# Kernel optimization log

Measured on AMD Instinct MI355X. Metric: run time of the kernel, lower is better.

## Reference

```python
import jax, jax.numpy as jnp
import numpy as np

BLOCK_SIZE = 256
N_EMBD = 384
NUM_BLOCKS = 3
N_HEADS = 6
VOCAB_SIZE = 65
HEAD = N_EMBD // N_HEADS
EPS = 1e-5


def setup_inputs() -> dict:
    key = jax.random.key(0)
    ks = jax.random.split(key, 20)
    B, T = 64, 256
    s = 0.02
    L = NUM_BLOCKS
    inp = {
        "idx": jax.random.randint(ks[0], (B, T), 0, VOCAB_SIZE),
        "tok_emb": jax.random.normal(ks[1], (VOCAB_SIZE, N_EMBD), jnp.float32) * s,
        "pos_emb": jax.random.normal(ks[2], (BLOCK_SIZE, N_EMBD), jnp.float32) * s,
        "Wq": jax.random.normal(ks[3], (L, N_EMBD, N_EMBD), jnp.float32) * s,
        "Wk": jax.random.normal(ks[4], (L, N_EMBD, N_EMBD), jnp.float32) * s,
        "Wv": jax.random.normal(ks[5], (L, N_EMBD, N_EMBD), jnp.float32) * s,
        "Wo": jax.random.normal(ks[6], (L, N_EMBD, N_EMBD), jnp.float32) * s,
        "bo": jnp.zeros((L, N_EMBD), jnp.float32),
        "ln1_g": jnp.ones((L, N_EMBD), jnp.float32),
        "ln1_b": jnp.zeros((L, N_EMBD), jnp.float32),
        "ln2_g": jnp.ones((L, N_EMBD), jnp.float32),
        "ln2_b": jnp.zeros((L, N_EMBD), jnp.float32),
        "W1": jax.random.normal(ks[7], (L, N_EMBD, 4 * N_EMBD), jnp.float32) * s,
        "b1": jnp.zeros((L, 4 * N_EMBD), jnp.float32),
        "W2": jax.random.normal(ks[8], (L, 4 * N_EMBD, N_EMBD), jnp.float32) * s,
        "b2": jnp.zeros((L, N_EMBD), jnp.float32),
        "lnf_g": jnp.ones((N_EMBD,), jnp.float32),
        "lnf_b": jnp.zeros((N_EMBD,), jnp.float32),
        "Wlm": jax.random.normal(ks[9], (N_EMBD, VOCAB_SIZE), jnp.float32) * s,
        "blm": jnp.zeros((VOCAB_SIZE,), jnp.float32),
    }
    return inp


def _ln(x, g, b):
    m = jnp.mean(x, axis=-1, keepdims=True)
    v = jnp.mean((x - m) ** 2, axis=-1, keepdims=True)
    return (x - m) * jax.lax.rsqrt(v + EPS) * g + b


def reference(idx, tok_emb, pos_emb, Wq, Wk, Wv, Wo, bo, ln1_g, ln1_b,
              ln2_g, ln2_b, W1, b1, W2, b2, lnf_g, lnf_b, Wlm, blm):
    B, T = idx.shape
    x = tok_emb[idx] + pos_emb[:T]  # [B,T,C]
    scale = N_EMBD ** (-0.5)  # NOTE: original scales by full C=N_EMBD, not head_size
    causal = jnp.tril(jnp.ones((T, T), bool))
    neg_inf = jnp.finfo(x.dtype).min
    for l in range(NUM_BLOCKS):
        h = _ln(x, ln1_g[l], ln1_b[l])
        q = (h @ Wq[l]).reshape(B, T, N_HEADS, HEAD)
        k = (h @ Wk[l]).reshape(B, T, N_HEADS, HEAD)
        v = (h @ Wv[l]).reshape(B, T, N_HEADS, HEAD)
        wei = jnp.einsum("bthd,bshd->bhts", q, k) * scale
        wei = jnp.where(causal, wei, neg_inf)
        wei = jax.nn.softmax(wei, axis=-1)  # dropout is identity in eval
        att = jnp.einsum("bhts,bshd->bthd", wei, v).reshape(B, T, N_EMBD)
        x = x + att @ Wo[l] + bo[l]
        h2 = _ln(x, ln2_g[l], ln2_b[l])
        x = x + jax.nn.relu(h2 @ W1[l] + b1[l]) @ W2[l] + b2[l]
    x = _ln(x, lnf_g, lnf_b)
    logits = x @ Wlm + blm  # [B,T,V]
    return logits
```

## Files before the change

kernel.cpp:

```cpp
#include <hip/hip_runtime.h>

#define Bb 64
#define Tt 256
#define Cc 384
#define Ll 3
#define Hh 6
#define HD 64
#define Vv 65
#define FF 1536
#define NT (Bb*Tt)
#define CQ 1152
#define LDP 72

typedef unsigned short u16;
typedef unsigned int   u32;
typedef __attribute__((ext_vector_type(8))) short bf16x8;
typedef __attribute__((ext_vector_type(4))) float f32x4;

__device__ __forceinline__ float bf2f(u16 u) {
    u32 v = ((u32)u) << 16; float f; __builtin_memcpy(&f, &v, 4); return f;
}
__device__ __forceinline__ u16 f2bf(float f) {
    u32 u; __builtin_memcpy(&u, &f, 4);
    u = (u + 0x7fffu + ((u >> 16) & 1u)) >> 16;
    return (u16)u;
}
__device__ __forceinline__ void gload16(const void* g, void* l) {
    __builtin_amdgcn_global_load_lds(
        (const __attribute__((address_space(1))) u32*)g,
        (__attribute__((address_space(3))) u32*)l, 16, 0, 0);
}

__global__ void k_embed(const int* __restrict__ idx, const float* __restrict__ tok,
                        const float* __restrict__ pos, float* __restrict__ x)
{
    long i = (long)blockIdx.x * 256 + threadIdx.x;
    if (i >= (long)NT * Cc) return;
    int c  = (int)(i % Cc);
    int bt = (int)(i / Cc);
    int t  = bt % Tt;
    x[i] = tok[idx[bt] * Cc + c] + pos[t * Cc + c];
}

__global__ __launch_bounds__(256) void k_ln(const float* __restrict__ x,
    const float* __restrict__ g, const float* __restrict__ b, u16* __restrict__ h)
{
    int row  = (int)((blockIdx.x * 256 + threadIdx.x) >> 6);
    int lane = threadIdx.x & 63;
    const float* xr = x + (long)row * Cc;
    float v[6]; float s = 0.f;
    #pragma unroll
    for (int j = 0; j < 6; ++j) { v[j] = xr[lane + 64 * j]; s += v[j]; }
    #pragma unroll
    for (int m = 32; m; m >>= 1) s += __shfl_xor(s, m, 64);
    float mean = s * (1.f / 384.f);
    float q = 0.f;
    #pragma unroll
    for (int j = 0; j < 6; ++j) { float d = v[j] - mean; q += d * d; }
    #pragma unroll
    for (int m = 32; m; m >>= 1) q += __shfl_xor(q, m, 64);
    float rstd = rsqrtf(q * (1.f / 384.f) + 1e-5f);
    u16* hr = h + (long)row * Cc;
    #pragma unroll
    for (int j = 0; j < 6; ++j) {
        int c = lane + 64 * j;
        hr[c] = f2bf((v[j] - mean) * rstd * g[c] + b[c]);
    }
}

__global__ __launch_bounds__(256) void k_cvtT_all(
    const float* __restrict__ Wq, const float* __restrict__ Wk,
    const float* __restrict__ Wv, const float* __restrict__ Wo,
    const float* __restrict__ W1, const float* __restrict__ W2,
    u16* __restrict__ Wqkvt, u16* __restrict__ Wot,
    u16* __restrict__ W1t, u16* __restrict__ W2t)
{
    int t = blockIdx.x;
    const float* src; u16* dst; int K, N, tt;
    if (t < 1728) {
        int m = t / 144; tt = t % 144; K = Cc; N = Cc;
        if (m < 9) {
            int l = m / 3, q = m % 3;
            src = (q == 0 ? Wq : q == 1 ? Wk : Wv) + (size_t)l * Cc * Cc;
            dst = Wqkvt + (size_t)l * CQ * Cc + (size_t)q * Cc * Cc;
        } else {
            int l = m - 9;
            src = Wo + (size_t)l * Cc * Cc;
            dst = Wot + (size_t)l * Cc * Cc;
        }
    } else if (t < 3456) {
        int u = t - 1728; int l = u / 576; tt = u % 576; K = Cc; N = FF;
        src = W1 + (size_t)l * Cc * FF; dst = W1t + (size_t)l * FF * Cc;
    } else {
        int u = t - 3456; int l = u / 576; tt = u % 576; K = FF; N = Cc;
        src = W2 + (size_t)l * FF * Cc; dst = W2t + (size_t)l * Cc * FF;
    }
    int nk = K / 32;
    int kt = (tt % nk) * 32, nt = (tt / nk) * 32;
    __shared__ u16 tile[32][33];
    int tx = threadIdx.x & 31, ty = threadIdx.x >> 5;
    #pragma unroll
    for (int r = 0; r < 4; ++r)
        tile[ty + 8 * r][tx] = f2bf(src[(long)(kt + ty + 8 * r) * N + nt + tx]);
    __syncthreads();
    #pragma unroll
    for (int r = 0; r < 4; ++r)
        dst[(long)(nt + ty + 8 * r) * K + kt + tx] = tile[tx][ty + 8 * r];
}

__global__ void k_cvtT_lm(const float* __restrict__ W, u16* __restrict__ Wt)
{
    int i = blockIdx.x * 256 + threadIdx.x;
    if (i >= 128 * Cc) return;
    int k = i % Cc, n = i / Cc;
    Wt[i] = (n < Vv) ? f2bf(W[(long)k * Vv + n]) : (u16)0;
}

template<int EPI>
__global__ __launch_bounds__(256) void k_gemm128(
    const u16* __restrict__ A, const u16* __restrict__ Bt,
    const float* __restrict__ bias, const float* __restrict__ R,
    void* __restrict__ Cout, int M, int N, int K, int Nout)
{
    __shared__ __align__(16) u16 As[128 * 64];
    __shared__ __align__(16) u16 Bs[128 * 64];
    const int bm = blockIdx.x * 128;
    const int bn = blockIdx.y * 128;
    const int tid = threadIdx.x;
    const int lane = tid & 63, w = tid >> 6;
    const int wr = w >> 1, wc = w & 1;
    const int l15 = lane & 15, g = lane >> 4;
    const int lr = lane >> 3;
    const int lc = ((lane & 7) ^ lr) * 8;

    f32x4 acc[4][4] = {};
    const u16* Ag = A  + (long)(bm + w * 32 + lr) * K + lc;
    const u16* Bg = Bt + (long)(bn + w * 32 + lr) * K + lc;
    u16* Ad = As + (w * 4) * 512;
    u16* Bd = Bs + (w * 4) * 512;

    for (int k0 = 0; k0 < K; k0 += 64) {
        #pragma unroll
        for (int s = 0; s < 4; ++s) {
            gload16(Ag + (long)s * 8 * K + k0, Ad + s * 512);
            gload16(Bg + (long)s * 8 * K + k0, Bd + s * 512);
        }
        __syncthreads();
        #pragma unroll
        for (int h = 0; h < 2; ++h) {
            const int cs = h * 4 + g;
            bf16x8 af[4], bfr[4];
            #pragma unroll
            for (int mi = 0; mi < 4; ++mi) {
                int row = wr * 64 + mi * 16 + l15;
                af[mi] = *(const bf16x8*)((const char*)As + row * 128 + ((cs ^ (row & 7)) << 4));
            }
            #pragma unroll
            for (int ni = 0; ni < 4; ++ni) {
                int row = wc * 64 + ni * 16 + l15;
                bfr[ni] = *(const bf16x8*)((const char*)Bs + row * 128 + ((cs ^ (row & 7)) << 4));
            }
            #pragma unroll
            for (int mi = 0; mi < 4; ++mi)
            #pragma unroll
            for (int ni = 0; ni < 4; ++ni)
                acc[mi][ni] = __builtin_amdgcn_mfma_f32_16x16x32_bf16(af[mi], bfr[ni], acc[mi][ni], 0, 0, 0);
        }
        __syncthreads();
    }
    #pragma unroll
    for (int mi = 0; mi < 4; ++mi)
    #pragma unroll
    for (int ni = 0; ni < 4; ++ni)
    #pragma unroll
    for (int i = 0; i < 4; ++i) {
        int row = bm + wr * 64 + mi * 16 + g * 4 + i;
        int col = bn + wc * 64 + ni * 16 + l15;
        float v = acc[mi][ni][i];
        if constexpr (EPI == 0) {
            ((u16*)Cout)[(long)row * N + col] = f2bf(v);
        } else if constexpr (EPI == 1) {
            v = fmaxf(v + bias[col], 0.f);
            ((u16*)Cout)[(long)row * N + col] = f2bf(v);
        } else if constexpr (EPI == 2) {
            long o = (long)row * N + col;
            ((float*)Cout)[o] = v + bias[col] + R[o];
        } else {
            if (col < Nout)
                ((float*)Cout)[(long)row * Nout + col] = v + bias[col];
        }
    }
}

template<int EPI>
__global__ __launch_bounds__(256) void k_gemm_n64(
    const u16* __restrict__ A, const u16* __restrict__ Bt,
    const float* __restrict__ bias, const float* __restrict__ R,
    void* __restrict__ Cout, int M, int N, int K, int Nout)
{
    __shared__ __align__(16) u16 As[128 * 64];
    __shared__ __align__(16) u16 Bs[64 * 64];
    const int bm = blockIdx.x * 128;
    const int bn = blockIdx.y * 64;
    const int tid = threadIdx.x;
    const int lane = tid & 63, w = tid >> 6;
    const int l15 = lane & 15, g = lane >> 4;
    const int lr = lane >> 3;
    const int lc = ((lane & 7) ^ lr) * 8;

    f32x4 acc[2][4] = {};
    const u16* Ag = A  + (long)(bm + w * 32 + lr) * K + lc;
    const u16* Bg = Bt + (long)(bn + w * 16 + lr) * K + lc;
    u16* Ad = As + (w * 4) * 512;
    u16* Bd = Bs + (w * 2) * 512;

    for (int k0 = 0; k0 < K; k0 += 64) {
        #pragma unroll
        for (int s = 0; s < 4; ++s)
            gload16(Ag + (long)s * 8 * K + k0, Ad + s * 512);
        #pragma unroll
        for (int t = 0; t < 2; ++t)
            gload16(Bg + (long)t * 8 * K + k0, Bd + t * 512);
        __syncthreads();
        #pragma unroll
        for (int h = 0; h < 2; ++h) {
            const int cs = h * 4 + g;
            bf16x8 af[2], bfr[4];
            #pragma unroll
            for (int mi = 0; mi < 2; ++mi) {
                int row = w * 32 + mi * 16 + l15;
                af[mi] = *(const bf16x8*)((const char*)As + row * 128 + ((cs ^ (row & 7)) << 4));
            }
            #pragma unroll
            for (int ni = 0; ni < 4; ++ni) {
                int row = ni * 16 + l15;
                bfr[ni] = *(const bf16x8*)((const char*)Bs + row * 128 + ((cs ^ (row & 7)) << 4));
            }
            #pragma unroll
            for (int mi = 0; mi < 2; ++mi)
            #pragma unroll
            for (int ni = 0; ni < 4; ++ni)
                acc[mi][ni] = __builtin_amdgcn_mfma_f32_16x16x32_bf16(af[mi], bfr[ni], acc[mi][ni], 0, 0, 0);
        }
        __syncthreads();
    }
    #pragma unroll
    for (int mi = 0; mi < 2; ++mi)
    #pragma unroll
    for (int ni = 0; ni < 4; ++ni)
    #pragma unroll
    for (int i = 0; i < 4; ++i) {
        int row = bm + w * 32 + mi * 16 + g * 4 + i;
        int col = bn + ni * 16 + l15;
        float v = acc[mi][ni][i];
        if constexpr (EPI == 0) {
            ((u16*)Cout)[(long)row * N + col] = f2bf(v);
        } else if constexpr (EPI == 1) {
            v = fmaxf(v + bias[col], 0.f);
            ((u16*)Cout)[(long)row * N + col] = f2bf(v);
        } else if constexpr (EPI == 2) {
            long o = (long)row * N + col;
            ((float*)Cout)[o] = v + bias[col] + R[o];
        } else {
            if (col < Nout)
                ((float*)Cout)[(long)row * Nout + col] = v + bias[col];
        }
    }
}

__global__ __launch_bounds__(256) void k_attn_mfma(const u16* __restrict__ qkv,
                                                   u16* __restrict__ att)
{
    __shared__ __align__(16) u16 ks[64][LDP];
    __shared__ __align__(16) u16 vt[64][LDP];
    __shared__ __align__(16) u16 pt[4][16][LDP];
    const int qt = blockIdx.x, hh = blockIdx.y, b = blockIdx.z;
    const int tid = threadIdx.x, lane = tid & 63, w = tid >> 6;
    const int l15 = lane & 15, g = lane >> 4;
    const int q0 = qt * 64;
    const long tokbase = (long)b * Tt;
    const float scale = 0.051031036307982884f;

    bf16x8 qa0, qa1;
    {
        const u16* qp = qkv + (tokbase + q0 + w * 16 + l15) * CQ + hh * HD + g * 8;
        qa0 = *(const bf16x8*)(qp);
        qa1 = *(const bf16x8*)(qp + 32);
    }
    f32x4 o[4] = {};
    float mrow[4] = {-1e30f, -1e30f, -1e30f, -1e30f};
    float lrow[4] = {0.f, 0.f, 0.f, 0.f};

    for (int kt = 0; kt <= qt; ++kt) {
        {
            int key = tid >> 2, c0 = (tid & 3) * 16;
            const u16* kg = qkv + (tokbase + kt * 64 + key) * CQ + Cc     + hh * HD + c0;
            const u16* vg = qkv + (tokbase + kt * 64 + key) * CQ + 2 * Cc + hh * HD + c0;
            *(bf16x8*)&ks[key][c0]     = *(const bf16x8*)kg;
            *(bf16x8*)&ks[key][c0 + 8] = *(const bf16x8*)(kg + 8);
            bf16x8 v0 = *(const bf16x8*)vg;
            bf16x8 v1 = *(const bf16x8*)(vg + 8);
            #pragma unroll
            for (int j = 0; j < 8; ++j) vt[c0 + j][key]     = (u16)v0[j];
            #pragma unroll
            for (int j = 0; j < 8; ++j) vt[c0 + 8 + j][key] = (u16)v1[j];
        }
        __syncthreads();
        f32x4 s[4] = {};
        #pragma unroll
        for (int c = 0; c < 4; ++c) {
            bf16x8 kb0 = *(const bf16x8*)&ks[c * 16 + l15][g * 8];
            bf16x8 kb1 = *(const bf16x8*)&ks[c * 16 + l15][32 + g * 8];
            s[c] = __builtin_amdgcn_mfma_f32_16x16x32_bf16(qa0, kb0, s[c], 0, 0, 0);
            s[c] = __builtin_amdgcn_mfma_f32_16x16x32_bf16(qa1, kb1, s[c], 0, 0, 0);
        }
        const bool diag = (kt == qt);
        #pragma unroll
        for (int c = 0; c < 4; ++c)
        #pragma unroll
        for (int i = 0; i < 4; ++i) {
            float v = s[c][i] * scale;
            if (diag && (c * 16 + l15 > w * 16 + 4 * g + i)) v = -1e30f;
            s[c][i] = v;
        }
        #pragma unroll
        for (int i = 0; i < 4; ++i) {
            float m0 = fmaxf(fmaxf(s[0][i], s[1][i]), fmaxf(s[2][i], s[3][i]));
            #pragma unroll
            for (int mm = 1; mm < 16; mm <<= 1) m0 = fmaxf(m0, __shfl_xor(m0, mm, 64));
            float mn = fmaxf(mrow[i], m0);
            float alpha = __expf(mrow[i] - mn);
            mrow[i] = mn;
            float sum = 0.f;
            #pragma unroll
            for (int c = 0; c < 4; ++c) {
                float p = __expf(s[c][i] - mn);
                s[c][i] = p;
                sum += p;
            }
            #pragma unroll
            for (int mm = 1; mm < 16; mm <<= 1) sum += __shfl_xor(sum, mm, 64);
            lrow[i] = lrow[i] * alpha + sum;
            #pragma unroll
            for (int d = 0; d < 4; ++d) o[d][i] *= alpha;
        }
        #pragma unroll
        for (int c = 0; c < 4; ++c)
        #pragma unroll
        for (int i = 0; i < 4; ++i)
            pt[w][g * 4 + i][c * 16 + l15] = f2bf(s[c][i]);
        bf16x8 pa0 = *(const bf16x8*)&pt[w][l15][g * 8];
        bf16x8 pa1 = *(const bf16x8*)&pt[w][l15][32 + g * 8];
        #pragma unroll
        for (int d = 0; d < 4; ++d) {
            bf16x8 vb0 = *(const bf16x8*)&vt[d * 16 + l15][g * 8];
            bf16x8 vb1 = *(const bf16x8*)&vt[d * 16 + l15][32 + g * 8];
            o[d] = __builtin_amdgcn_mfma_f32_16x16x32_bf16(pa0, vb0, o[d], 0, 0, 0);
            o[d] = __builtin_amdgcn_mfma_f32_16x16x32_bf16(pa1, vb1, o[d], 0, 0, 0);
        }
        __syncthreads();
    }
    #pragma unroll
    for (int i = 0; i < 4; ++i) {
        float inv = 1.f / lrow[i];
        int row = q0 + w * 16 + g * 4 + i;
        u16* ap = att + (tokbase + row) * Cc + hh * HD;
        #pragma unroll
        for (int d = 0; d < 4; ++d)
            ap[d * 16 + l15] = f2bf(o[d][i] * inv);
    }
}

extern "C" void kernel_launch(void* const* d_in, const int* in_sizes, int n_in,
                              void* d_out, int out_size, void* d_ws, size_t ws_size,
                              hipStream_t stream)
{
    (void)in_sizes; (void)n_in; (void)out_size; (void)ws_size;
    const int*   idx  = (const int*)d_in[0];
    const float* tok  = (const float*)d_in[1];
    const float* pos  = (const float*)d_in[2];
    const float* Wq   = (const float*)d_in[3];
    const float* Wk   = (const float*)d_in[4];
    const float* Wv   = (const float*)d_in[5];
    const float* Wo   = (const float*)d_in[6];
    const float* bo   = (const float*)d_in[7];
    const float* ln1g = (const float*)d_in[8];
    const float* ln1b = (const float*)d_in[9];
    const float* ln2g = (const float*)d_in[10];
    const float* ln2b = (const float*)d_in[11];
    const float* W1   = (const float*)d_in[12];
    const float* b1   = (const float*)d_in[13];
    const float* W2   = (const float*)d_in[14];
    const float* b2   = (const float*)d_in[15];
    const float* lnfg = (const float*)d_in[16];
    const float* lnfb = (const float*)d_in[17];
    const float* Wlm  = (const float*)d_in[18];
    const float* blm  = (const float*)d_in[19];

    char* w = (char*)d_ws;
    auto carve = [&](size_t bytes) { char* p = w; w += (bytes + 255) & ~(size_t)255; return p; };
    float* x   = (float*)carve((size_t)NT * Cc * 4);
    u16*  big  = (u16*)carve((size_t)NT * FF * 2);
    u16*  h    = (u16*)carve((size_t)NT * Cc * 2);
    u16*  ab   = (u16*)carve((size_t)NT * Cc * 2);
    u16*  Wqkvt= (u16*)carve((size_t)Ll * CQ * Cc * 2);
    u16*  Wot  = (u16*)carve((size_t)Ll * Cc * Cc * 2);
    u16*  W1t  = (u16*)carve((size_t)Ll * FF * Cc * 2);
    u16*  W2t  = (u16*)carve((size_t)Ll * Cc * FF * 2);
    u16*  Wlmt = (u16*)carve((size_t)128 * Cc * 2);
    u16*  qkvb = big;
    u16*  fb   = big;

    const int TPB = 256;
    k_cvtT_all<<<5184, TPB, 0, stream>>>(Wq, Wk, Wv, Wo, W1, W2, Wqkvt, Wot, W1t, W2t);
    k_cvtT_lm<<<(128 * Cc + 255) / 256, TPB, 0, stream>>>(Wlm, Wlmt);
    k_embed<<<((long)NT * Cc + 255) / 256, TPB, 0, stream>>>(idx, tok, pos, x);

    for (int l = 0; l < Ll; ++l) {
        k_ln<<<NT / 4, TPB, 0, stream>>>(x, ln1g + l * Cc, ln1b + l * Cc, h);
        k_gemm128<0><<<dim3(NT / 128, CQ / 128), TPB, 0, stream>>>(
            h, Wqkvt + (size_t)l * CQ * Cc, nullptr, nullptr, qkvb, NT, CQ, Cc, CQ);
        k_attn_mfma<<<dim3(4, Hh, Bb), TPB, 0, stream>>>(qkvb, ab);
        k_gemm_n64<2><<<dim3(NT / 128, Cc / 64), TPB, 0, stream>>>(
            ab, Wot + (size_t)l * Cc * Cc, bo + l * Cc, x, x, NT, Cc, Cc, Cc);
        k_ln<<<NT / 4, TPB, 0, stream>>>(x, ln2g + l * Cc, ln2b + l * Cc, h);
        k_gemm128<1><<<dim3(NT / 128, FF / 128), TPB, 0, stream>>>(
            h, W1t + (size_t)l * FF * Cc, b1 + l * FF, nullptr, fb, NT, FF, Cc, FF);
        k_gemm_n64<2><<<dim3(NT / 128, Cc / 64), TPB, 0, stream>>>(
            fb, W2t + (size_t)l * Cc * FF, b2 + l * Cc, x, x, NT, Cc, FF, Cc);
    }
    k_ln<<<NT / 4, TPB, 0, stream>>>(x, lnfg, lnfb, h);
    k_gemm_n64<3><<<dim3(NT / 128, 2), TPB, 0, stream>>>(
        h, Wlmt, blm, nullptr, (float*)d_out, NT, 128, Cc, Vv);
}
```

Baseline: 462.8 us.

## Double-buffer GEMM shared tiles and stage epilogues through LDS for vector stores

```diff
diff --git a/kernel.cpp b/kernel.cpp
--- a/kernel.cpp
+++ b/kernel.cpp
@@ -119,11 +119,10 @@
 template<int EPI>
 __global__ __launch_bounds__(256) void k_gemm128(
     const u16* __restrict__ A, const u16* __restrict__ Bt,
-    const float* __restrict__ bias, const float* __restrict__ R,
-    void* __restrict__ Cout, int M, int N, int K, int Nout)
-{
-    __shared__ __align__(16) u16 As[128 * 64];
-    __shared__ __align__(16) u16 Bs[128 * 64];
+    const float* __restrict__ bias, void* __restrict__ Cout, int M, int N, int K)
+{
+    __shared__ __align__(16) u16 As[2][128 * 64];
+    __shared__ __align__(16) u16 Bs[2][128 * 64];
     const int bm = blockIdx.x * 128;
     const int bn = blockIdx.y * 128;
     const int tid = threadIdx.x;
@@ -136,16 +135,21 @@
     f32x4 acc[4][4] = {};
     const u16* Ag = A  + (long)(bm + w * 32 + lr) * K + lc;
     const u16* Bg = Bt + (long)(bn + w * 32 + lr) * K + lc;
-    u16* Ad = As + (w * 4) * 512;
-    u16* Bd = Bs + (w * 4) * 512;
-
-    for (int k0 = 0; k0 < K; k0 += 64) {
+
+    auto stage = [&](int buf, int k0) {
+        u16* Ad = As[buf] + (w * 4) * 512;
+        u16* Bd = Bs[buf] + (w * 4) * 512;
         #pragma unroll
         for (int s = 0; s < 4; ++s) {
             gload16(Ag + (long)s * 8 * K + k0, Ad + s * 512);
             gload16(Bg + (long)s * 8 * K + k0, Bd + s * 512);
         }
-        __syncthreads();
+    };
+    stage(0, 0);
+    __syncthreads();
+    int cur = 0;
+    for (int k0 = 0; k0 < K; k0 += 64) {
+        if (k0 + 64 < K) stage(cur ^ 1, k0 + 64);
         #pragma unroll
         for (int h = 0; h < 2; ++h) {
             const int cs = h * 4 + g;
@@ -153,12 +157,12 @@
             #pragma unroll
             for (int mi = 0; mi < 4; ++mi) {
                 int row = wr * 64 + mi * 16 + l15;
-                af[mi] = *(const bf16x8*)((const char*)As + row * 128 + ((cs ^ (row & 7)) << 4));
+                af[mi] = *(const bf16x8*)((const char*)As[cur] + row * 128 + ((cs ^ (row & 7)) << 4));
             }
             #pragma unroll
             for (int ni = 0; ni < 4; ++ni) {
                 int row = wc * 64 + ni * 16 + l15;
-                bfr[ni] = *(const bf16x8*)((const char*)Bs + row * 128 + ((cs ^ (row & 7)) << 4));
+                bfr[ni] = *(const bf16x8*)((const char*)Bs[cur] + row * 128 + ((cs ^ (row & 7)) << 4));
             }
             #pragma unroll
             for (int mi = 0; mi < 4; ++mi)
@@ -167,28 +171,29 @@
                 acc[mi][ni] = __builtin_amdgcn_mfma_f32_16x16x32_bf16(af[mi], bfr[ni], acc[mi][ni], 0, 0, 0);
         }
         __syncthreads();
-    }
+        cur ^= 1;
+    }
+    u16* cb = &As[0][0];
     #pragma unroll
     for (int mi = 0; mi < 4; ++mi)
     #pragma unroll
     for (int ni = 0; ni < 4; ++ni)
     #pragma unroll
     for (int i = 0; i < 4; ++i) {
-        int row = bm + wr * 64 + mi * 16 + g * 4 + i;
-        int col = bn + wc * 64 + ni * 16 + l15;
+        int row = wr * 64 + mi * 16 + g * 4 + i;
+        int col = wc * 64 + ni * 16 + l15;
         float v = acc[mi][ni][i];
-        if constexpr (EPI == 0) {
-            ((u16*)Cout)[(long)row * N + col] = f2bf(v);
-        } else if constexpr (EPI == 1) {
-            v = fmaxf(v + bias[col], 0.f);
-            ((u16*)Cout)[(long)row * N + col] = f2bf(v);
-        } else if constexpr (EPI == 2) {
-            long o = (long)row * N + col;
-            ((float*)Cout)[o] = v + bias[col] + R[o];
-        } else {
-            if (col < Nout)
-                ((float*)Cout)[(long)row * Nout + col] = v + bias[col];
-        }
+        if constexpr (EPI == 1) v = fmaxf(v + bias[bn + col], 0.f);
+        *(u16*)((char*)cb + row * 256 + ((((col >> 3) ^ (row & 7))) << 4) + (col & 7) * 2) = f2bf(v);
+    }
+    __syncthreads();
+    u16* Cg = (u16*)Cout;
+    #pragma unroll
+    for (int p = 0; p < 8; ++p) {
+        int row = p * 16 + (tid >> 4);
+        int slot = (tid & 15) ^ (row & 7);
+        bf16x8 val = *(const bf16x8*)((const char*)cb + row * 256 + (slot << 4));
+        *(bf16x8*)&Cg[(long)(bm + row) * N + bn + (tid & 15) * 8] = val;
     }
 }
 
@@ -198,8 +203,8 @@
     const float* __restrict__ bias, const float* __restrict__ R,
     void* __restrict__ Cout, int M, int N, int K, int Nout)
 {
-    __shared__ __align__(16) u16 As[128 * 64];
-    __shared__ __align__(16) u16 Bs[64 * 64];
+    __shared__ __align__(16) u16 As[2][128 * 64];
+    __shared__ __align__(16) u16 Bs[2][64 * 64];
     const int bm = blockIdx.x * 128;
     const int bn = blockIdx.y * 64;
     const int tid = threadIdx.x;
@@ -211,17 +216,22 @@
     f32x4 acc[2][4] = {};
     const u16* Ag = A  + (long)(bm + w * 32 + lr) * K + lc;
     const u16* Bg = Bt + (long)(bn + w * 16 + lr) * K + lc;
-    u16* Ad = As + (w * 4) * 512;
-    u16* Bd = Bs + (w * 2) * 512;
-
-    for (int k0 = 0; k0 < K; k0 += 64) {
+
+    auto stage = [&](int buf, int k0) {
+        u16* Ad = As[buf] + (w * 4) * 512;
+        u16* Bd = Bs[buf] + (w * 2) * 512;
         #pragma unroll
         for (int s = 0; s < 4; ++s)
             gload16(Ag + (long)s * 8 * K + k0, Ad + s * 512);
         #pragma unroll
         for (int t = 0; t < 2; ++t)
             gload16(Bg + (long)t * 8 * K + k0, Bd + t * 512);
-        __syncthreads();
+    };
+    stage(0, 0);
+    __syncthreads();
+    int cur = 0;
+    for (int k0 = 0; k0 < K; k0 += 64) {
+        if (k0 + 64 < K) stage(cur ^ 1, k0 + 64);
         #pragma unroll
         for (int h = 0; h < 2; ++h) {
             const int cs = h * 4 + g;
@@ -229,12 +239,12 @@
             #pragma unroll
             for (int mi = 0; mi < 2; ++mi) {
                 int row = w * 32 + mi * 16 + l15;
-                af[mi] = *(const bf16x8*)((const char*)As + row * 128 + ((cs ^ (row & 7)) << 4));
+                af[mi] = *(const bf16x8*)((const char*)As[cur] + row * 128 + ((cs ^ (row & 7)) << 4));
             }
             #pragma unroll
             for (int ni = 0; ni < 4; ++ni) {
                 int row = ni * 16 + l15;
-                bfr[ni] = *(const bf16x8*)((const char*)Bs + row * 128 + ((cs ^ (row & 7)) << 4));
+                bfr[ni] = *(const bf16x8*)((const char*)Bs[cur] + row * 128 + ((cs ^ (row & 7)) << 4));
             }
             #pragma unroll
             for (int mi = 0; mi < 2; ++mi)
@@ -243,27 +253,43 @@
                 acc[mi][ni] = __builtin_amdgcn_mfma_f32_16x16x32_bf16(af[mi], bfr[ni], acc[mi][ni], 0, 0, 0);
         }
         __syncthreads();
-    }
-    #pragma unroll
-    for (int mi = 0; mi < 2; ++mi)
-    #pragma unroll
-    for (int ni = 0; ni < 4; ++ni)
-    #pragma unroll
-    for (int i = 0; i < 4; ++i) {
-        int row = bm + w * 32 + mi * 16 + g * 4 + i;
-        int col = bn + ni * 16 + l15;
-        float v = acc[mi][ni][i];
-        if constexpr (EPI == 0) {
-            ((u16*)Cout)[(long)row * N + col] = f2bf(v);
-        } else if constexpr (EPI == 1) {
-            v = fmaxf(v + bias[col], 0.f);
-            ((u16*)Cout)[(long)row * N + col] = f2bf(v);
-        } else if constexpr (EPI == 2) {
-            long o = (long)row * N + col;
-            ((float*)Cout)[o] = v + bias[col] + R[o];
-        } else {
+        cur ^= 1;
+    }
+    if constexpr (EPI == 2) {
+        float* cb = (float*)&As[0][0];
+        #pragma unroll
+        for (int mi = 0; mi < 2; ++mi)
+        #pragma unroll
+        for (int ni = 0; ni < 4; ++ni)
+        #pragma unroll
+        for (int i = 0; i < 4; ++i) {
+            int row = w * 32 + mi * 16 + g * 4 + i;
+            int col = ni * 16 + l15;
+            float v = acc[mi][ni][i] + bias[bn + col];
+            *(float*)((char*)cb + row * 256 + ((((col >> 2) ^ (row & 7))) << 4) + (col & 3) * 4) = v;
+        }
+        __syncthreads();
+        float* Cg = (float*)Cout;
+        #pragma unroll
+        for (int p = 0; p < 8; ++p) {
+            int row = p * 16 + (tid >> 4);
+            int slot = (tid & 15) ^ (row & 7);
+            f32x4 val = *(const f32x4*)((const char*)cb + row * 256 + (slot << 4));
+            long o = (long)(bm + row) * N + bn + (tid & 15) * 4;
+            f32x4 r = *(const f32x4*)&R[o];
+            *(f32x4*)&Cg[o] = val + r;
+        }
+    } else {
+        #pragma unroll
+        for (int mi = 0; mi < 2; ++mi)
+        #pragma unroll
+        for (int ni = 0; ni < 4; ++ni)
+        #pragma unroll
+        for (int i = 0; i < 4; ++i) {
+            int row = bm + w * 32 + mi * 16 + g * 4 + i;
+            int col = bn + ni * 16 + l15;
             if (col < Nout)
-                ((float*)Cout)[(long)row * Nout + col] = v + bias[col];
+                ((float*)Cout)[(long)row * Nout + col] = acc[mi][ni][i] + bias[col];
         }
     }
 }
@@ -419,13 +445,13 @@
     for (int l = 0; l < Ll; ++l) {
         k_ln<<<NT / 4, TPB, 0, stream>>>(x, ln1g + l * Cc, ln1b + l * Cc, h);
         k_gemm128<0><<<dim3(NT / 128, CQ / 128), TPB, 0, stream>>>(
-            h, Wqkvt + (size_t)l * CQ * Cc, nullptr, nullptr, qkvb, NT, CQ, Cc, CQ);
+            h, Wqkvt + (size_t)l * CQ * Cc, nullptr, qkvb, NT, CQ, Cc);
         k_attn_mfma<<<dim3(4, Hh, Bb), TPB, 0, stream>>>(qkvb, ab);
         k_gemm_n64<2><<<dim3(NT / 128, Cc / 64), TPB, 0, stream>>>(
             ab, Wot + (size_t)l * Cc * Cc, bo + l * Cc, x, x, NT, Cc, Cc, Cc);
         k_ln<<<NT / 4, TPB, 0, stream>>>(x, ln2g + l * Cc, ln2b + l * Cc, h);
         k_gemm128<1><<<dim3(NT / 128, FF / 128), TPB, 0, stream>>>(
-            h, W1t + (size_t)l * FF * Cc, b1 + l * FF, nullptr, fb, NT, FF, Cc, FF);
+            h, W1t + (size_t)l * FF * Cc, b1 + l * FF, fb, NT, FF, Cc);
         k_gemm_n64<2><<<dim3(NT / 128, Cc / 64), TPB, 0, stream>>>(
             fb, W2t + (size_t)l * Cc * FF, b2 + l * Cc, x, x, NT, Cc, FF, Cc);
     }
```

Result: slower. 483.6 us (+4.5%).
